# Kernel tuning notes

Hardware: AMD Instinct MI355X
Metric: run time of the kernel (lower is better)

The kernel has to match this reference:

```python
import jax, jax.numpy as jnp
import numpy as np


def _chamfer_pair(x, y):
    # x: [N,3], y: [M,3] -> per-point squared NN distances (dist1 [N], dist2 [M])
    # d_ij = |x_i|^2 + |y_j|^2 - 2 x_i . y_j
    d = (jnp.sum(x * x, axis=1)[:, None]
         + jnp.sum(y * y, axis=1)[None, :]
         - 2.0 * (x @ y.T))  # [N, M]
    return jnp.min(d, axis=1), jnp.min(d, axis=0)


def setup_inputs() -> dict:
    key = jax.random.key(0)
    k1, k2 = jax.random.split(key)
    B, N, M = 4, 8192, 8192
    xyz1 = jax.random.normal(k1, (B, N, 3), dtype=jnp.float32)
    xyz2 = jax.random.normal(k2, (B, M, 3), dtype=jnp.float32)
    return {"xyz1": xyz1, "xyz2": xyz2}


def reference(xyz1, xyz2):
    # lax.map over batch keeps peak memory to one [N,M] matrix at a time,
    # mirroring the tiled custom-kernel structure of ChamferFunction.
    dist1, dist2 = jax.lax.map(lambda ab: _chamfer_pair(ab[0], ab[1]), (xyz1, xyz2))
    return jnp.mean(dist1) + jnp.mean(dist2)
```

## Files before the change

kernel.cpp:

```cpp
#include <hip/hip_runtime.h>


#define BATCH 4
#define NPTS 8192
#define TPB 256
#define NFRAG 4
#define COLS_PER_WAVE 128
#define COLS_PER_BLOCK 512
#define XBLKS (NPTS / COLS_PER_BLOCK)
#define YSEGS 8
#define YSEG (NPTS / YSEGS)
#define CHUNK 512
#define NCHUNK (YSEG / CHUNK)
#define JT (CHUNK / 32)

typedef __attribute__((ext_vector_type(8))) short bf16x8;
typedef __attribute__((ext_vector_type(16))) float f32x16;
union FragU { int4 i4; bf16x8 v; };

__device__ inline unsigned short bf16_rne(float f) {
    unsigned int u = __float_as_uint(f);
    return (unsigned short)((u + 0x7FFFu + ((u >> 16) & 1u)) >> 16);
}
__device__ inline float bf16_f32(unsigned short h) {
    return __uint_as_float(((unsigned int)h) << 16);
}
__device__ inline unsigned int pack2(unsigned int lo, unsigned int hi) {
    return (lo & 0xFFFFu) | (hi << 16);
}

__global__ __launch_bounds__(256) void prepack_kernel(
    const float* __restrict__ xyz1, const float* __restrict__ xyz2,
    int4* __restrict__ rowpack, int4* __restrict__ colpack)
{
    const int id  = blockIdx.x * 256 + threadIdx.x;
    const int arr = id >> 15;
    const int rem = id & 32767;
    const float* p = (arr ? xyz2 : xyz1) + (size_t)rem * 3;
    const float x0 = p[0], x1 = p[1], x2 = p[2];

    const unsigned short h0 = bf16_rne(x0), h1 = bf16_rne(x1), h2 = bf16_rne(x2);
    const unsigned short l0 = bf16_rne(x0 - bf16_f32(h0));
    const unsigned short l1 = bf16_rne(x1 - bf16_f32(h1));
    const unsigned short l2 = bf16_rne(x2 - bf16_f32(h2));
    const float s = x0 * x0 + x1 * x1 + x2 * x2;
    const unsigned short sh = bf16_rne(s);
    const unsigned short sl = bf16_rne(s - bf16_f32(sh));
    const unsigned short one = 0x3F80;

    int4 rlo, rhi;
    rlo.x = pack2(h0, h1); rlo.y = pack2(h2, h0);
    rlo.z = pack2(h1, h2); rlo.w = pack2(l0, l1);
    rhi.x = pack2(l2, one); rhi.y = pack2(one, sh);
    rhi.z = pack2(sl, 0u);  rhi.w = 0;
    rowpack[2 * id]     = rlo;
    rowpack[2 * id + 1] = rhi;

    const float g0 = -2.0f * x0, g1 = -2.0f * x1, g2 = -2.0f * x2;
    const unsigned short gh0 = bf16_rne(g0), gh1 = bf16_rne(g1), gh2 = bf16_rne(g2);
    const unsigned short gl0 = bf16_rne(g0 - bf16_f32(gh0));
    const unsigned short gl1 = bf16_rne(g1 - bf16_f32(gh1));
    const unsigned short gl2 = bf16_rne(g2 - bf16_f32(gh2));
    int4 clo, chi;
    clo.x = pack2(gh0, gh1); clo.y = pack2(gh2, gl0);
    clo.z = pack2(gl1, gl2); clo.w = pack2(gh0, gh1);
    chi.x = pack2(gh2, sh);  chi.y = pack2(sl, one);
    chi.z = pack2(one, 0u);  chi.w = 0;
    colpack[2 * id]     = clo;
    colpack[2 * id + 1] = chi;
}

__device__ inline float red16(float cb, const f32x16& d) {
    const float m0 = fminf(fminf(d[0],  d[1]),  d[2]);
    const float m1 = fminf(fminf(d[3],  d[4]),  d[5]);
    const float m2 = fminf(fminf(d[6],  d[7]),  d[8]);
    const float m3 = fminf(fminf(d[9],  d[10]), d[11]);
    const float m4 = fminf(fminf(d[12], d[13]), d[14]);
    const float u0 = fminf(fminf(m0, m1), m2);
    const float u1 = fminf(fminf(m3, m4), d[15]);
    return fminf(fminf(cb, u0), u1);
}

__global__ __launch_bounds__(TPB, 4) void chamfer_main(
    const int4* __restrict__ rowpack,
    const int4* __restrict__ colpack,
    unsigned int* __restrict__ keys)
{
    const int blk  = blockIdx.x;
    const int seg  = blk & (YSEGS - 1);
    const int xblk = (blk >> 3) & (XBLKS - 1);
    const int b    = (blk >> 7) & (BATCH - 1);
    const int dir  = blk >> 9;
    const int arrB = dir;
    const int arrA = dir ^ 1;

    const int t = threadIdx.x, lane = t & 63, wave = t >> 6;
    const int half = lane >> 5, l31 = lane & 31;

    __shared__ int4 sb0[CHUNK];
    __shared__ int4 sb1[CHUNK];

    const int xbase = xblk * COLS_PER_BLOCK + wave * COLS_PER_WAVE;
    const size_t cb_idx = ((size_t)(arrB * BATCH + b) * NPTS + xbase) * 2;
    FragU bf0, bf1, bf2, bf3;
    bf0.i4 = colpack[cb_idx + (size_t)(0 * 32 + l31) * 2 + half];
    bf1.i4 = colpack[cb_idx + (size_t)(1 * 32 + l31) * 2 + half];
    bf2.i4 = colpack[cb_idx + (size_t)(2 * 32 + l31) * 2 + half];
    bf3.i4 = colpack[cb_idx + (size_t)(3 * 32 + l31) * 2 + half];

    float cb[NFRAG];
#pragma unroll
    for (int f = 0; f < NFRAG; ++f) cb[f] = __builtin_inff();
    const f32x16 zero = {0.0f, 0.0f, 0.0f, 0.0f, 0.0f, 0.0f, 0.0f, 0.0f,
                         0.0f, 0.0f, 0.0f, 0.0f, 0.0f, 0.0f, 0.0f, 0.0f};

    const size_t rbase = ((size_t)(arrA * BATCH + b) * NPTS + (size_t)seg * YSEG) * 2;

    for (int c = 0; c < NCHUNK; ++c) {
        __syncthreads();
        {
            const int4* src = rowpack + rbase + (size_t)c * CHUNK * 2 + (size_t)t * 4;
            const int4 a0 = src[0], a1 = src[1], a2 = src[2], a3 = src[3];
            sb0[2 * t]     = a0;  sb1[2 * t]     = a1;
            sb0[2 * t + 1] = a2;  sb1[2 * t + 1] = a3;
        }
        __syncthreads();

        const int4* asrc = half ? sb1 : sb0;
#pragma unroll 2
        for (int jt = 0; jt < JT; ++jt) {
            FragU af; af.i4 = asrc[jt * 32 + l31];
            f32x16 d0 = __builtin_amdgcn_mfma_f32_32x32x16_bf16(af.v, bf0.v, zero, 0, 0, 0);
            f32x16 d1 = __builtin_amdgcn_mfma_f32_32x32x16_bf16(af.v, bf1.v, zero, 0, 0, 0);
            f32x16 d2 = __builtin_amdgcn_mfma_f32_32x32x16_bf16(af.v, bf2.v, zero, 0, 0, 0);
            f32x16 d3 = __builtin_amdgcn_mfma_f32_32x32x16_bf16(af.v, bf3.v, zero, 0, 0, 0);
            asm volatile("" :: "v"(d0));
            asm volatile("" :: "v"(d1));
            asm volatile("" :: "v"(d2));
            asm volatile("" :: "v"(d3));
            cb[0] = red16(cb[0], d0);
            cb[1] = red16(cb[1], d1);
            cb[2] = red16(cb[2], d2);
            cb[3] = red16(cb[3], d3);
        }
    }

    unsigned int* ok = keys + ((size_t)dir * BATCH + b) * NPTS + xbase;
#pragma unroll
    for (int f = 0; f < NFRAG; ++f) {
        const float v = fminf(cb[f], __shfl_xor(cb[f], 32, 64));
        if (half == 0) {
            const unsigned int u = __float_as_uint(v);
            const unsigned int key = u ^ ((u >> 31) ? 0xFFFFFFFFu : 0x80000000u);
            atomicMin(&ok[f * 32 + l31], key);
        }
    }
}

__device__ inline float key_decode(unsigned int key) {
    const unsigned int u = (key & 0x80000000u) ? (key ^ 0x80000000u) : ~key;
    return __uint_as_float(u);
}

__global__ __launch_bounds__(1024) void reduce_kernel(
    const unsigned int* __restrict__ u1,
    const unsigned int* __restrict__ u2,
    float* __restrict__ out)
{
    const int n4 = BATCH * NPTS / 4;
    const uint4* v1 = (const uint4*)u1;
    const uint4* v2 = (const uint4*)u2;
    double s1 = 0.0, s2 = 0.0;
    for (int i = threadIdx.x; i < n4; i += blockDim.x) {
        const uint4 a = v1[i];
        const uint4 c = v2[i];
        s1 += (double)key_decode(a.x) + (double)key_decode(a.y)
            + (double)key_decode(a.z) + (double)key_decode(a.w);
        s2 += (double)key_decode(c.x) + (double)key_decode(c.y)
            + (double)key_decode(c.z) + (double)key_decode(c.w);
    }
    for (int off = 32; off > 0; off >>= 1) {
        s1 += __shfl_down(s1, off, 64);
        s2 += __shfl_down(s2, off, 64);
    }
    __shared__ double l1[16], l2[16];
    const int wave = threadIdx.x >> 6;
    if ((threadIdx.x & 63) == 0) { l1[wave] = s1; l2[wave] = s2; }
    __syncthreads();
    if (threadIdx.x == 0) {
        double t1 = 0.0, t2 = 0.0;
        const int nw = blockDim.x >> 6;
        for (int w = 0; w < nw; ++w) { t1 += l1[w]; t2 += l2[w]; }
        const double n = (double)(BATCH * NPTS);
        out[0] = (float)(t1 / n + t2 / n);
    }
}

extern "C" void kernel_launch(void* const* d_in, const int* in_sizes, int n_in,
                              void* d_out, int out_size, void* d_ws, size_t ws_size,
                              hipStream_t stream) {
    const float* xyz1 = (const float*)d_in[0];
    const float* xyz2 = (const float*)d_in[1];
    float* out = (float*)d_out;

    int4* rowpack = (int4*)d_ws;
    int4* colpack = rowpack + 2 * 65536;
    unsigned int* keys = (unsigned int*)(colpack + 2 * 65536);

    hipMemsetAsync(keys, 0xFF, 2 * BATCH * NPTS * sizeof(unsigned int), stream);
    prepack_kernel<<<256, 256, 0, stream>>>(xyz1, xyz2, rowpack, colpack);

    chamfer_main<<<2 * BATCH * XBLKS * YSEGS, TPB, 0, stream>>>(rowpack, colpack, keys);

    reduce_kernel<<<1, 1024, 0, stream>>>(keys, keys + BATCH * NPTS, out);
}
```

Baseline: 37.09 us.

## Halve per-wave column tile, fold memset into prepack, parallelize final reduction

The main kernel now gives each wave 2 column fragments instead of 4. That doubles the block count and raises the occupancy target to 8 blocks per CU, in exchange for twice the shared-memory row loads per output. The separate memset is removed: prepack initializes the keys and a counter. The single-block reduction becomes 8 blocks that write partial sums, and the last block to finish, found through an atomic counter, combines them. This cuts launch and serial-reduction overhead but adds a cross-block atomic handshake.

```diff
diff --git a/kernel.cpp b/kernel.cpp
--- a/kernel.cpp
+++ b/kernel.cpp
@@ -4,9 +4,9 @@
 #define BATCH 4
 #define NPTS 8192
 #define TPB 256
-#define NFRAG 4
-#define COLS_PER_WAVE 128
-#define COLS_PER_BLOCK 512
+#define NFRAG 2
+#define COLS_PER_WAVE 64
+#define COLS_PER_BLOCK 256
 #define XBLKS (NPTS / COLS_PER_BLOCK)
 #define YSEGS 8
 #define YSEG (NPTS / YSEGS)
@@ -31,13 +31,17 @@
 
 __global__ __launch_bounds__(256) void prepack_kernel(
     const float* __restrict__ xyz1, const float* __restrict__ xyz2,
-    int4* __restrict__ rowpack, int4* __restrict__ colpack)
+    int4* __restrict__ rowpack, int4* __restrict__ colpack,
+    unsigned int* __restrict__ keys, unsigned int* __restrict__ counter)
 {
     const int id  = blockIdx.x * 256 + threadIdx.x;
     const int arr = id >> 15;
     const int rem = id & 32767;
     const float* p = (arr ? xyz2 : xyz1) + (size_t)rem * 3;
     const float x0 = p[0], x1 = p[1], x2 = p[2];
+
+    keys[id] = 0xFFFFFFFFu;
+    if (id == 0) *counter = 0;
 
     const unsigned short h0 = bf16_rne(x0), h1 = bf16_rne(x1), h2 = bf16_rne(x2);
     const unsigned short l0 = bf16_rne(x0 - bf16_f32(h0));
@@ -81,7 +85,7 @@
     return fminf(fminf(cb, u0), u1);
 }
 
-__global__ __launch_bounds__(TPB, 4) void chamfer_main(
+__global__ __launch_bounds__(TPB, 8) void chamfer_main(
     const int4* __restrict__ rowpack,
     const int4* __restrict__ colpack,
     unsigned int* __restrict__ keys)
@@ -89,8 +93,8 @@
     const int blk  = blockIdx.x;
     const int seg  = blk & (YSEGS - 1);
     const int xblk = (blk >> 3) & (XBLKS - 1);
-    const int b    = (blk >> 7) & (BATCH - 1);
-    const int dir  = blk >> 9;
+    const int b    = (blk >> 8) & (BATCH - 1);
+    const int dir  = blk >> 10;
     const int arrB = dir;
     const int arrA = dir ^ 1;
 
@@ -102,11 +106,9 @@
 
     const int xbase = xblk * COLS_PER_BLOCK + wave * COLS_PER_WAVE;
     const size_t cb_idx = ((size_t)(arrB * BATCH + b) * NPTS + xbase) * 2;
-    FragU bf0, bf1, bf2, bf3;
+    FragU bf0, bf1;
     bf0.i4 = colpack[cb_idx + (size_t)(0 * 32 + l31) * 2 + half];
     bf1.i4 = colpack[cb_idx + (size_t)(1 * 32 + l31) * 2 + half];
-    bf2.i4 = colpack[cb_idx + (size_t)(2 * 32 + l31) * 2 + half];
-    bf3.i4 = colpack[cb_idx + (size_t)(3 * 32 + l31) * 2 + half];
 
     float cb[NFRAG];
 #pragma unroll
@@ -127,21 +129,14 @@
         __syncthreads();
 
         const int4* asrc = half ? sb1 : sb0;
-#pragma unroll 2
+#pragma unroll 4
         for (int jt = 0; jt < JT; ++jt) {
             FragU af; af.i4 = asrc[jt * 32 + l31];
             f32x16 d0 = __builtin_amdgcn_mfma_f32_32x32x16_bf16(af.v, bf0.v, zero, 0, 0, 0);
             f32x16 d1 = __builtin_amdgcn_mfma_f32_32x32x16_bf16(af.v, bf1.v, zero, 0, 0, 0);
-            f32x16 d2 = __builtin_amdgcn_mfma_f32_32x32x16_bf16(af.v, bf2.v, zero, 0, 0, 0);
-            f32x16 d3 = __builtin_amdgcn_mfma_f32_32x32x16_bf16(af.v, bf3.v, zero, 0, 0, 0);
-            asm volatile("" :: "v"(d0));
-            asm volatile("" :: "v"(d1));
-            asm volatile("" :: "v"(d2));
-            asm volatile("" :: "v"(d3));
+            asm volatile("" :: "v"(d0), "v"(d1));
             cb[0] = red16(cb[0], d0);
             cb[1] = red16(cb[1], d1);
-            cb[2] = red16(cb[2], d2);
-            cb[3] = red16(cb[3], d3);
         }
     }
 
@@ -163,22 +158,20 @@
 }
 
 __global__ __launch_bounds__(1024) void reduce_kernel(
-    const unsigned int* __restrict__ u1,
-    const unsigned int* __restrict__ u2,
+    const unsigned int* __restrict__ keys,
+    unsigned long long* __restrict__ partials,
+    unsigned int* __restrict__ counter,
     float* __restrict__ out)
 {
-    const int n4 = BATCH * NPTS / 4;
-    const uint4* v1 = (const uint4*)u1;
-    const uint4* v2 = (const uint4*)u2;
-    double s1 = 0.0, s2 = 0.0;
-    for (int i = threadIdx.x; i < n4; i += blockDim.x) {
-        const uint4 a = v1[i];
-        const uint4 c = v2[i];
-        s1 += (double)key_decode(a.x) + (double)key_decode(a.y)
-            + (double)key_decode(a.z) + (double)key_decode(a.w);
-        s2 += (double)key_decode(c.x) + (double)key_decode(c.y)
-            + (double)key_decode(c.z) + (double)key_decode(c.w);
-    }
+    const uint4* v1 = (const uint4*)keys;
+    const uint4* v2 = (const uint4*)(keys + BATCH * NPTS);
+    const int idx = blockIdx.x * 1024 + threadIdx.x;
+    const uint4 a = v1[idx];
+    const uint4 c = v2[idx];
+    double s1 = (double)key_decode(a.x) + (double)key_decode(a.y)
+              + (double)key_decode(a.z) + (double)key_decode(a.w);
+    double s2 = (double)key_decode(c.x) + (double)key_decode(c.y)
+              + (double)key_decode(c.z) + (double)key_decode(c.w);
     for (int off = 32; off > 0; off >>= 1) {
         s1 += __shfl_down(s1, off, 64);
         s2 += __shfl_down(s2, off, 64);
@@ -189,10 +182,20 @@
     __syncthreads();
     if (threadIdx.x == 0) {
         double t1 = 0.0, t2 = 0.0;
-        const int nw = blockDim.x >> 6;
-        for (int w = 0; w < nw; ++w) { t1 += l1[w]; t2 += l2[w]; }
-        const double n = (double)(BATCH * NPTS);
-        out[0] = (float)(t1 / n + t2 / n);
+        for (int w = 0; w < 16; ++w) { t1 += l1[w]; t2 += l2[w]; }
+        atomicExch(&partials[2 * blockIdx.x],     (unsigned long long)__double_as_longlong(t1));
+        atomicExch(&partials[2 * blockIdx.x + 1], (unsigned long long)__double_as_longlong(t2));
+        __threadfence();
+        const unsigned int old = atomicAdd(counter, 1u);
+        if (old == 7u) {
+            double g1 = 0.0, g2 = 0.0;
+            for (int w = 0; w < 8; ++w) {
+                g1 += __longlong_as_double((long long)atomicAdd(&partials[2 * w],     0ull));
+                g2 += __longlong_as_double((long long)atomicAdd(&partials[2 * w + 1], 0ull));
+            }
+            const double n = (double)(BATCH * NPTS);
+            out[0] = (float)(g1 / n + g2 / n);
+        }
     }
 }
 
@@ -206,11 +209,12 @@
     int4* rowpack = (int4*)d_ws;
     int4* colpack = rowpack + 2 * 65536;
     unsigned int* keys = (unsigned int*)(colpack + 2 * 65536);
-
-    hipMemsetAsync(keys, 0xFF, 2 * BATCH * NPTS * sizeof(unsigned int), stream);
-    prepack_kernel<<<256, 256, 0, stream>>>(xyz1, xyz2, rowpack, colpack);
+    unsigned long long* partials = (unsigned long long*)(keys + 2 * BATCH * NPTS);
+    unsigned int* counter = (unsigned int*)(partials + 16);
+
+    prepack_kernel<<<256, 256, 0, stream>>>(xyz1, xyz2, rowpack, colpack, keys, counter);
 
     chamfer_main<<<2 * BATCH * XBLKS * YSEGS, TPB, 0, stream>>>(rowpack, colpack, keys);
 
-    reduce_kernel<<<1, 1024, 0, stream>>>(keys, keys + BATCH * NPTS, out);
-}
+    reduce_kernel<<<8, 1024, 0, stream>>>(keys, partials, counter, out);
+}
```

After: 33.45 us. -9.8%, faster.
